# Kernel optimization log

Hardware: AMD Instinct MI355X
Metric: run time of the kernel (lower is better)

The kernel has to match this reference:

```python
import jax, jax.numpy as jnp
import numpy as np
from math import sqrt

B, N, CS, H, D, K = 8, 256, 512, 8, 64, 32
NB = 2 * K + 1          # no_bins = 65
CT = 2048               # c_transition
INF = 1e9
WL = sqrt(0.5)          # w_L
EPS = 1e-5


def setup_inputs() -> dict:
    key = jax.random.key(0)
    ks = jax.random.split(key, 10)
    sc = 0.02
    return {
        "s": jax.random.normal(ks[0], (B, N, CS), jnp.float32),
        "masks": jnp.ones((B, N), jnp.bool_),
        "wq": jax.random.normal(ks[1], (CS, D * H), jnp.float32) * sc,
        "wk": jax.random.normal(ks[2], (CS, D * H), jnp.float32) * sc,
        "wv": jax.random.normal(ks[3], (CS, D * H), jnp.float32) * sc,
        "wb": jax.random.normal(ks[4], (NB, H), jnp.float32) * sc,
        "wo": jax.random.normal(ks[5], ((NB + D) * H, CS), jnp.float32) * sc,
        "bo": jnp.zeros((CS,), jnp.float32),
        "ln1_g": jnp.ones((CS,), jnp.float32),
        "ln1_b": jnp.zeros((CS,), jnp.float32),
        "w1": jax.random.normal(ks[6], (CS, CT), jnp.float32) * sc,
        "b1": jnp.zeros((CT,), jnp.float32),
        "w2": jax.random.normal(ks[7], (CT, CS), jnp.float32) * sc,
        "b2": jnp.zeros((CS,), jnp.float32),
        "ln2_g": jnp.ones((CS,), jnp.float32),
        "ln2_b": jnp.zeros((CS,), jnp.float32),
    }


def _layernorm(x, g, b):
    m = jnp.mean(x, -1, keepdims=True)
    v = jnp.var(x, -1, keepdims=True)
    return (x - m) * jax.lax.rsqrt(v + EPS) * g + b


def _heads(x):  # [B,N,D*H] -> [B,H,N,D]  (torch: reshape(B,N,D,H) then move H forward)
    return jnp.transpose(x.reshape(B, N, D, H), (0, 3, 1, 2))


def reference(s, masks, wq, wk, wv, wb, wo, bo, ln1_g, ln1_b, w1, b1, w2, b2, ln2_g, ln2_b):
    mf = masks.astype(s.dtype)                       # [B,N]
    sq = mf[:, :, None] * mf[:, None, :]             # [B,N,N]

    # relative position one-hot, clipped to [-K, K] -> [N,N,NB]
    r = jnp.arange(N)
    dmat = jnp.clip(r[:, None] - r[None, :], -K, K) + K
    relpos_base = jax.nn.one_hot(dmat, NB, dtype=s.dtype)
    relpos = relpos_base[None] * sq[..., None]       # [B,N,N,NB]

    b_bias = jnp.einsum('bijc,ch->bhij', relpos, wb)  # [B,H,N,N]

    q = _heads(s @ wq)                               # [B,H,N,D]
    k = _heads(s @ wk)
    v = _heads(s @ wv)

    logits = WL * (jnp.einsum('bhid,bhjd->bhij', q, k) / sqrt(D) + b_bias)
    logits = logits - INF * (1.0 - sq)[:, None]      # mask
    a = jax.nn.softmax(logits, axis=-1)              # [B,H,N,N]

    # pairwise aggregation and value aggregation (einsum avoids [B,H,N,N,NB] blowup)
    o_pair = jnp.einsum('bhij,bijc->bhic', a, relpos)  # [B,H,N,NB]
    o = jnp.einsum('bhij,bhjd->bhid', a, v)            # [B,H,N,D]

    op = jnp.transpose(o_pair, (0, 2, 1, 3)).reshape(B, N, H * NB)
    ov = jnp.transpose(o, (0, 2, 1, 3)).reshape(B, N, H * D)
    embd = jnp.concatenate([op, ov], axis=-1) @ wo + bo   # [B,N,CS]

    x = _layernorm(s + embd, ln1_g, ln1_b)
    ff = jax.nn.relu(x @ w1 + b1) @ w2 + b2
    x = _layernorm(x + ff, ln2_g, ln2_b)
    return x, a
```

## Files before the change

### kernel.cpp

```cpp
#include <hip/hip_runtime.h>
#include <hip/hip_bf16.h>
#include <cstdint>

#define B_ 8
#define N_ 256
#define CS_ 512
#define H_ 8
#define D_ 64
#define K_ 32
#define NB_ 65
#define CT_ 2048
#define WL_ 0.70710678118654752f

typedef __attribute__((ext_vector_type(8))) short bf16x8;
typedef __attribute__((ext_vector_type(4))) float f32x4;

#define GLOBAL_AS __attribute__((address_space(1)))
#define LDS_AS __attribute__((address_space(3)))

__device__ __forceinline__ void async16(void* lds, const void* g) {
  __builtin_amdgcn_global_load_lds((const GLOBAL_AS uint32_t*)g,
                                   (LDS_AS uint32_t*)lds, 16, 0, 0);
}

__device__ __forceinline__ ushort f2bf(float v) {
  __hip_bfloat16 hb = __float2bfloat16(v);
  return *(ushort*)&hb;
}

__global__ __launch_bounds__(256) void gemm_bf16(
    const ushort* __restrict__ A, const ushort* __restrict__ Bt,
    const float* __restrict__ bias, float* __restrict__ C,
    ushort* __restrict__ Cb, int M, int Nc, int Kd, int flags) {
  __shared__ ushort As[128 * 64];
  __shared__ ushort Bs[128 * 64];
  int tid = threadIdx.x;
  int bm = blockIdx.y * 128, bn = blockIdx.x * 128;
  int S = gridDim.z, z = blockIdx.z;
  int T = Kd >> 6;
  int it0 = (z * T) / S, it1 = ((z + 1) * T) / S;
  if (flags & 8) C += (size_t)z * M * Nc;
  int w = tid >> 6, l = tid & 63;
  int wr = (w >> 1) * 64, wc = (w & 1) * 64;
  int lm = l & 15, lq = l >> 4;
  int srow = tid >> 3;
  int sg = tid & 7;

  f32x4 acc[4][4];
#pragma unroll
  for (int i = 0; i < 4; ++i)
#pragma unroll
    for (int j = 0; j < 4; ++j) acc[i][j] = (f32x4){0.f, 0.f, 0.f, 0.f};

  for (int it = it0; it < it1; ++it) {
    int k0 = it << 6;
    __syncthreads();
#pragma unroll
    for (int r = 0; r < 4; ++r) {
      int row = r * 32 + srow;
      int gl = sg ^ (row & 7);
      async16(&As[row * 64 + sg * 8],
              A + (size_t)(bm + row) * Kd + k0 + gl * 8);
      async16(&Bs[row * 64 + sg * 8],
              Bt + (size_t)(bn + row) * Kd + k0 + gl * 8);
    }
    __syncthreads();
#pragma unroll
    for (int kk = 0; kk < 2; ++kk) {
      bf16x8 af[4], bfr[4];
#pragma unroll
      for (int i = 0; i < 4; ++i) {
        int ma = wr + 16 * i + lm;
        af[i] = *(const bf16x8*)&As[ma * 64 + ((kk * 4 + lq) ^ (ma & 7)) * 8];
        int nb = wc + 16 * i + lm;
        bfr[i] = *(const bf16x8*)&Bs[nb * 64 + ((kk * 4 + lq) ^ (nb & 7)) * 8];
      }
#pragma unroll
      for (int i = 0; i < 4; ++i)
#pragma unroll
        for (int j = 0; j < 4; ++j)
          acc[i][j] = __builtin_amdgcn_mfma_f32_16x16x32_bf16(
              af[i], bfr[j], acc[i][j], 0, 0, 0);
    }
  }
#pragma unroll
  for (int j = 0; j < 4; ++j) {
    int col = bn + wc + 16 * j + lm;
    float bv = ((flags & 1) && z == 0) ? bias[col] : 0.f;
#pragma unroll
    for (int i = 0; i < 4; ++i) {
#pragma unroll
      for (int r = 0; r < 4; ++r) {
        int row = bm + wr + 16 * i + lq * 4 + r;
        float v = acc[i][j][r] + bv;
        if (flags & 2) v = fmaxf(v, 0.f);
        if (flags & 8) C[(size_t)row * Nc + col] = v;
        if (flags & 4) Cb[(size_t)row * Nc + col] = f2bf(v);
        if (flags & 16) {
          int which = col >> 9, c = col & 511;
          int hh = c >> 6, d2 = c & 63;
          int bb = row >> 8, nn = row & 255;
          size_t dst;
          if (which == 2)
            dst = (size_t)2 * 1048576 + (((size_t)(bb * 8 + hh) * 64) + d2) * 256 + nn;
          else
            dst = (size_t)which * 1048576 + (((size_t)(bb * 8 + hh) * 256) + nn) * 64 + d2;
          Cb[dst] = f2bf(v);
        }
      }
    }
  }
}

__global__ __launch_bounds__(256) void prep_all(
    const float* __restrict__ s, __hip_bfloat16* __restrict__ s_bf,
    const float* __restrict__ wq, const float* __restrict__ wk,
    const float* __restrict__ wv, const float* __restrict__ wo,
    const float* __restrict__ w1, const float* __restrict__ w2,
    __hip_bfloat16* __restrict__ wqkvT, __hip_bfloat16* __restrict__ wopT,
    __hip_bfloat16* __restrict__ w1T, __hip_bfloat16* __restrict__ w2T) {
  int blk = blockIdx.x;
  if (blk < 1024) {
    int i = blk * 256 + threadIdx.x;
    float4 v = ((const float4*)s)[i];
    s_bf[i * 4 + 0] = __float2bfloat16(v.x);
    s_bf[i * 4 + 1] = __float2bfloat16(v.y);
    s_bf[i * 4 + 2] = __float2bfloat16(v.z);
    s_bf[i * 4 + 3] = __float2bfloat16(v.w);
    return;
  }
  blk -= 1024;
  __shared__ float tile[32][33];
  const float* src;
  __hip_bfloat16* dst;
  int R, C, Kpad, tX, tIdx, whichBase = -1;
  if (blk < 768) {
    int zz = blk >> 8; tIdx = blk & 255;
    src = zz == 0 ? wq : zz == 1 ? wk : wv;
    dst = wqkvT; whichBase = zz * 512; R = 512; C = 512; Kpad = 512; tX = 16;
  } else if (blk < 1312) {
    tIdx = blk - 768; src = wo; dst = wopT; R = 1032; C = 512; Kpad = 1088; tX = 16;
  } else if (blk < 2336) {
    tIdx = blk - 1312; src = w1; dst = w1T; R = 512; C = 2048; Kpad = 512; tX = 64;
  } else {
    tIdx = blk - 2336; src = w2; dst = w2T; R = 2048; C = 512; Kpad = 2048; tX = 16;
  }
  int c0 = (tIdx % tX) * 32, r0 = (tIdx / tX) * 32;
  int tx = threadIdx.x & 31, ty = threadIdx.x >> 5;
#pragma unroll
  for (int yy = 0; yy < 32; yy += 8) {
    int r = r0 + ty + yy, c = c0 + tx;
    tile[ty + yy][tx] = (r < R && c < C) ? src[(size_t)r * C + c] : 0.f;
  }
  __syncthreads();
#pragma unroll
  for (int yy = 0; yy < 32; yy += 8) {
    int cc = c0 + ty + yy, k = r0 + tx;
    if (cc < C && k < Kpad) {
      int n = (whichBase >= 0) ? (whichBase + (cc & 7) * 64 + (cc >> 3)) : cc;
      dst[(size_t)n * Kpad + k] = __float2bfloat16(tile[tx][ty + yy]);
    }
  }
}

__global__ __launch_bounds__(256) void attn_fused(
    const ushort* __restrict__ qh, const ushort* __restrict__ kh,
    const ushort* __restrict__ vT, const int* __restrict__ masks,
    const float* __restrict__ wb, float* __restrict__ a_out,
    ushort* __restrict__ cat) {
  int strip = blockIdx.x & 3, bh = blockIdx.x >> 2;
  int h = bh & 7, b = bh >> 3;
  __shared__ ushort lds[20480];
  __shared__ float wbs[NB_];
  __shared__ float mfj[256];
  ushort* Ks = lds;
  ushort* Qs = lds + 16384;
  ushort* Vh = lds;
  ushort* Ps = lds + 8192;
  int tid = threadIdx.x;
  int srow = tid >> 3, sg = tid & 7;
#pragma unroll
  for (int rr = 0; rr < 8; ++rr) {
    int row = rr * 32 + srow;
    int gl = sg ^ (row & 7);
    async16(&Ks[row * 64 + sg * 8],
            kh + ((size_t)bh * 256 + row) * 64 + gl * 8);
  }
#pragma unroll
  for (int rr = 0; rr < 2; ++rr) {
    int row = rr * 32 + srow;
    int gl = sg ^ (row & 7);
    async16(&Qs[row * 64 + sg * 8],
            qh + ((size_t)bh * 256 + strip * 64 + row) * 64 + gl * 8);
  }
  if (tid < NB_) wbs[tid] = wb[tid * H_ + h];
  mfj[tid] = (masks[b * 256 + tid] != 0) ? 1.f : 0.f;
  __syncthreads();

  int w = tid >> 6, l = tid & 63, lm = l & 15, lq = l >> 4;
  bf16x8 qf[2];
#pragma unroll
  for (int kk = 0; kk < 2; ++kk) {
    int qrow = w * 16 + lm;
    qf[kk] = *(const bf16x8*)&Qs[qrow * 64 + ((kk * 4 + lq) ^ (qrow & 7)) * 8];
  }
  f32x4 acc[16];
#pragma unroll
  for (int ct = 0; ct < 16; ++ct) {
    int krow = ct * 16 + lm;
    bf16x8 kf0 = *(const bf16x8*)&Ks[krow * 64 + ((lq) ^ (krow & 7)) * 8];
    bf16x8 kf1 = *(const bf16x8*)&Ks[krow * 64 + ((4 + lq) ^ (krow & 7)) * 8];
    f32x4 zf = (f32x4){0.f, 0.f, 0.f, 0.f};
    zf = __builtin_amdgcn_mfma_f32_16x16x32_bf16(qf[0], kf0, zf, 0, 0, 0);
    acc[ct] = __builtin_amdgcn_mfma_f32_16x16x32_bf16(qf[1], kf1, zf, 0, 0, 0);
  }
  int ibase = strip * 64 + w * 16 + lq * 4;
  float mfi[4];
#pragma unroll
  for (int r = 0; r < 4; ++r) mfi[r] = mfj[ibase + r];
#pragma unroll
  for (int ct = 0; ct < 16; ++ct) {
    int j = ct * 16 + lm;
    float mj = mfj[j];
#pragma unroll
    for (int r = 0; r < 4; ++r) {
      int i = ibase + r;
      int diff = i - j;
      int cb = diff < -K_ ? 0 : (diff > K_ ? 2 * K_ : diff + K_);
      float sq = mfi[r] * mj;
      acc[ct][r] = WL_ * (acc[ct][r] * 0.125f + wbs[cb] * sq) - 1e9f * (1.f - sq);
    }
  }
  float mx[4], sm[4];
#pragma unroll
  for (int r = 0; r < 4; ++r) {
    float m = acc[0][r];
#pragma unroll
    for (int ct = 1; ct < 16; ++ct) m = fmaxf(m, acc[ct][r]);
#pragma unroll
    for (int o = 1; o < 16; o <<= 1) m = fmaxf(m, __shfl_xor(m, o, 64));
    mx[r] = m;
  }
#pragma unroll
  for (int ct = 0; ct < 16; ++ct)
#pragma unroll
    for (int r = 0; r < 4; ++r) acc[ct][r] = __expf(acc[ct][r] - mx[r]);
#pragma unroll
  for (int r = 0; r < 4; ++r) {
    float s = 0.f;
#pragma unroll
    for (int ct = 0; ct < 16; ++ct) s += acc[ct][r];
#pragma unroll
    for (int o = 1; o < 16; o <<= 1) s += __shfl_xor(s, o, 64);
    sm[r] = 1.f / s;
  }
  float p0[4] = {0.f, 0.f, 0.f, 0.f}, p64[4] = {0.f, 0.f, 0.f, 0.f};
#pragma unroll
  for (int ct = 0; ct < 16; ++ct) {
    int j = ct * 16 + lm;
    float mj = mfj[j];
#pragma unroll
    for (int r = 0; r < 4; ++r) {
      int i = ibase + r;
      float aval = acc[ct][r] * sm[r];
      a_out[((size_t)bh * 256 + i) * 256 + j] = aval;
      float val = aval * mfi[r] * mj;
      int diff = i - j;
      if (diff <= -K_)      p0[r] += val;
      else if (diff >= K_)  p64[r] += val;
      else cat[((size_t)(b * 256 + i)) * 1088 + h * 65 + diff + K_] = f2bf(val);
    }
  }
#pragma unroll
  for (int r = 0; r < 4; ++r)
#pragma unroll
    for (int o = 1; o < 16; o <<= 1) {
      p0[r]  += __shfl_xor(p0[r], o, 64);
      p64[r] += __shfl_xor(p64[r], o, 64);
    }
  if (lm == 0) {
#pragma unroll
    for (int r = 0; r < 4; ++r) {
      int i = ibase + r;
      cat[((size_t)(b * 256 + i)) * 1088 + h * 65 + 0]      = f2bf(p0[r]);
      cat[((size_t)(b * 256 + i)) * 1088 + h * 65 + 2 * K_] = f2bf(p64[r]);
    }
  }
#pragma unroll
  for (int r = 0; r < 4; ++r) {
    int i = ibase + r;
#pragma unroll
    for (int t = 0; t < 4; ++t) {
      int c = 1 + lm + 16 * t;
      if (c < 64) {
        int j = i - c + K_;
        if (j < 0 || j > 255)
          cat[((size_t)(b * 256 + i)) * 1088 + h * 65 + c] = 0;
      }
    }
  }
  if (h == 0) {
    for (int idx = tid; idx < 64 * 56; idx += 256) {
      int r = idx / 56, c = 1032 + idx - r * 56 * 1 - (idx / 56) * 0;
      c = 1032 + (idx - r * 56);
      cat[((size_t)(b * 256 + strip * 64 + r)) * 1088 + c] = 0;
    }
  }
  __syncthreads();
  f32x4 acc2[4];
#pragma unroll
  for (int nt = 0; nt < 4; ++nt) acc2[nt] = (f32x4){0.f, 0.f, 0.f, 0.f};
  int vrow_ = tid >> 4, vsg = tid & 15;
#pragma unroll
  for (int hf = 0; hf < 2; ++hf) {
    if (hf == 1) __syncthreads();
#pragma unroll
    for (int rr = 0; rr < 4; ++rr) {
      int d = rr * 16 + vrow_;
      int gl = vsg ^ (d & 7);
      async16(&Vh[d * 128 + vsg * 8],
              vT + (size_t)bh * 16384 + d * 256 + hf * 128 + gl * 8);
    }
#pragma unroll
    for (int cl = 0; cl < 8; ++cl) {
      int ct = hf * 8 + cl;
#pragma unroll
      for (int r = 0; r < 4; ++r) {
        int rowl = w * 16 + lq * 4 + r;
        float aval = acc[ct][r] * sm[r];
        int g = cl * 2 + (lm >> 3);
        Ps[rowl * 128 + ((g ^ (rowl & 7)) << 3) + (lm & 7)] = f2bf(aval);
      }
    }
    __syncthreads();
#pragma unroll
    for (int kst = 0; kst < 4; ++kst) {
      int prow = w * 16 + lm;
      bf16x8 af = *(const bf16x8*)&Ps[prow * 128 + (((kst * 4 + lq) ^ (prow & 7)) << 3)];
#pragma unroll
      for (int nt = 0; nt < 4; ++nt) {
        int d = nt * 16 + lm;
        bf16x8 bfr = *(const bf16x8*)&Vh[d * 128 + (((kst * 4 + lq) ^ (d & 7)) << 3)];
        acc2[nt] = __builtin_amdgcn_mfma_f32_16x16x32_bf16(af, bfr, acc2[nt], 0, 0, 0);
      }
    }
  }
#pragma unroll
  for (int nt = 0; nt < 4; ++nt) {
    int d = nt * 16 + lm;
#pragma unroll
    for (int r = 0; r < 4; ++r) {
      int i = ibase + r;
      cat[((size_t)(b * 256 + i)) * 1088 + 520 + h * 64 + d] = f2bf(acc2[nt][r]);
    }
  }
}

__device__ __forceinline__ float lnReduceSum(float v, float* red) {
#pragma unroll
  for (int o = 32; o > 0; o >>= 1) v += __shfl_xor(v, o, 64);
  int w = threadIdx.x >> 6;
  __syncthreads();
  if ((threadIdx.x & 63) == 0) red[w] = v;
  __syncthreads();
  return red[0] + red[1] + red[2] + red[3];
}

__global__ __launch_bounds__(256) void ln_sum(
    const float* __restrict__ x1, const float* __restrict__ xp,
    int S, int stride, const float* __restrict__ g,
    const float* __restrict__ bta, float* __restrict__ out,
    __hip_bfloat16* __restrict__ out_bf) {
  __shared__ float red[4];
  int row = blockIdx.x, tid = threadIdx.x;
  size_t base = (size_t)row * 512;
  float v0 = x1[base + tid];
  float v1 = x1[base + tid + 256];
  for (int s = 0; s < S; ++s) {
    v0 += xp[(size_t)s * stride + base + tid];
    v1 += xp[(size_t)s * stride + base + tid + 256];
  }
  float su = lnReduceSum(v0 + v1, red);
  float sq = lnReduceSum(v0 * v0 + v1 * v1, red);
  float mean = su * (1.f / 512.f);
  float var = sq * (1.f / 512.f) - mean * mean;
  float inv = rsqrtf(var + 1e-5f);
  float o0 = (v0 - mean) * inv * g[tid] + bta[tid];
  float o1 = (v1 - mean) * inv * g[tid + 256] + bta[tid + 256];
  out[base + tid]       = o0;
  out[base + tid + 256] = o1;
  if (out_bf) {
    out_bf[base + tid]       = __float2bfloat16(o0);
    out_bf[base + tid + 256] = __float2bfloat16(o1);
  }
}

extern "C" void kernel_launch(void* const* d_in, const int* in_sizes, int n_in,
                              void* d_out, int out_size, void* d_ws, size_t ws_size,
                              hipStream_t stream) {
  const float* s     = (const float*)d_in[0];
  const int*   masks = (const int*)d_in[1];
  const float* wq = (const float*)d_in[2];
  const float* wk = (const float*)d_in[3];
  const float* wv = (const float*)d_in[4];
  const float* wb = (const float*)d_in[5];
  const float* wo = (const float*)d_in[6];
  const float* bo = (const float*)d_in[7];
  const float* ln1_g = (const float*)d_in[8];
  const float* ln1_b = (const float*)d_in[9];
  const float* w1 = (const float*)d_in[10];
  const float* b1 = (const float*)d_in[11];
  const float* w2 = (const float*)d_in[12];
  const float* b2 = (const float*)d_in[13];
  const float* ln2_g = (const float*)d_in[14];
  const float* ln2_b = (const float*)d_in[15];

  float* out_x = (float*)d_out;
  float* out_a = out_x + 1048576;

  float* ws = (float*)d_ws;
  float* embd_part = ws + 0;
  float* xbuf      = ws + 4194304;
  float* ff_part   = ws + 5242880;
  ushort* qkv_bf   = (ushort*)(ws + 9437184);
  ushort* q_bf = qkv_bf;
  ushort* k_bf = qkv_bf + 1048576;
  ushort* v_bf = qkv_bf + 2097152;
  ushort* cat_bf = (ushort*)(ws + 10223616);
  __hip_bfloat16* h_bf  = (__hip_bfloat16*)(ws + 11337728);
  __hip_bfloat16* s_bf  = (__hip_bfloat16*)(ws + 13434880);
  __hip_bfloat16* x_bf  = (__hip_bfloat16*)(ws + 13959168);
  __hip_bfloat16* wqkvT = (__hip_bfloat16*)(ws + 14483456);
  __hip_bfloat16* wopT  = (__hip_bfloat16*)(ws + 14876672);
  __hip_bfloat16* w1T   = (__hip_bfloat16*)(ws + 15155200);
  __hip_bfloat16* w2T   = (__hip_bfloat16*)(ws + 15679488);

  dim3 blk(256);
  prep_all<<<dim3(4384), blk, 0, stream>>>(s, s_bf, wq, wk, wv, wo, w1, w2,
                                           wqkvT, wopT, w1T, w2T);
  gemm_bf16<<<dim3(12, 16, 1), blk, 0, stream>>>(
      (const ushort*)s_bf, (const ushort*)wqkvT, nullptr, nullptr,
      qkv_bf, 2048, 1536, 512, 16);
  attn_fused<<<dim3(256), blk, 0, stream>>>(q_bf, k_bf, v_bf, masks, wb,
                                            out_a, cat_bf);
  gemm_bf16<<<dim3(4, 16, 4), blk, 0, stream>>>(
      cat_bf, (const ushort*)wopT, bo, embd_part, nullptr,
      2048, 512, 1088, 1 | 8);
  ln_sum<<<dim3(2048), blk, 0, stream>>>(s, embd_part, 4, 1048576,
                                         ln1_g, ln1_b, xbuf, x_bf);
  gemm_bf16<<<dim3(16, 16, 1), blk, 0, stream>>>(
      (const ushort*)x_bf, (const ushort*)w1T, b1, nullptr, (ushort*)h_bf,
      2048, 2048, 512, 1 | 2 | 4);
  gemm_bf16<<<dim3(4, 16, 4), blk, 0, stream>>>(
      (const ushort*)h_bf, (const ushort*)w2T, b2, ff_part, nullptr,
      2048, 512, 2048, 1 | 8);
  ln_sum<<<dim3(2048), blk, 0, stream>>>(xbuf, ff_part, 4, 1048576,
                                         ln2_g, ln2_b, out_x, nullptr);
}
```

Baseline: 197.1 us.

## Shrink GEMM tiles to 64x128 with two waves; load Q/V fragments directly into registers

```diff
diff --git a/kernel.cpp b/kernel.cpp
--- a/kernel.cpp
+++ b/kernel.cpp
@@ -28,20 +28,19 @@
   return *(ushort*)&hb;
 }
 
-__global__ __launch_bounds__(256) void gemm_bf16(
+__global__ __launch_bounds__(128) void gemm_bf16(
     const ushort* __restrict__ A, const ushort* __restrict__ Bt,
     const float* __restrict__ bias, float* __restrict__ C,
     ushort* __restrict__ Cb, int M, int Nc, int Kd, int flags) {
-  __shared__ ushort As[128 * 64];
+  __shared__ ushort As[64 * 64];
   __shared__ ushort Bs[128 * 64];
   int tid = threadIdx.x;
-  int bm = blockIdx.y * 128, bn = blockIdx.x * 128;
+  int bm = blockIdx.y * 64, bn = blockIdx.x * 128;
   int S = gridDim.z, z = blockIdx.z;
   int T = Kd >> 6;
   int it0 = (z * T) / S, it1 = ((z + 1) * T) / S;
   if (flags & 8) C += (size_t)z * M * Nc;
   int w = tid >> 6, l = tid & 63;
-  int wr = (w >> 1) * 64, wc = (w & 1) * 64;
   int lm = l & 15, lq = l >> 4;
   int srow = tid >> 3;
   int sg = tid & 7;
@@ -57,10 +56,15 @@
     __syncthreads();
 #pragma unroll
     for (int r = 0; r < 4; ++r) {
-      int row = r * 32 + srow;
+      int row = r * 16 + srow;
       int gl = sg ^ (row & 7);
       async16(&As[row * 64 + sg * 8],
               A + (size_t)(bm + row) * Kd + k0 + gl * 8);
+    }
+#pragma unroll
+    for (int r = 0; r < 8; ++r) {
+      int row = r * 16 + srow;
+      int gl = sg ^ (row & 7);
       async16(&Bs[row * 64 + sg * 8],
               Bt + (size_t)(bn + row) * Kd + k0 + gl * 8);
     }
@@ -70,9 +74,9 @@
       bf16x8 af[4], bfr[4];
 #pragma unroll
       for (int i = 0; i < 4; ++i) {
-        int ma = wr + 16 * i + lm;
+        int ma = 16 * i + lm;
         af[i] = *(const bf16x8*)&As[ma * 64 + ((kk * 4 + lq) ^ (ma & 7)) * 8];
-        int nb = wc + 16 * i + lm;
+        int nb = w * 64 + 16 * i + lm;
         bfr[i] = *(const bf16x8*)&Bs[nb * 64 + ((kk * 4 + lq) ^ (nb & 7)) * 8];
       }
 #pragma unroll
@@ -85,13 +89,13 @@
   }
 #pragma unroll
   for (int j = 0; j < 4; ++j) {
-    int col = bn + wc + 16 * j + lm;
+    int col = bn + w * 64 + 16 * j + lm;
     float bv = ((flags & 1) && z == 0) ? bias[col] : 0.f;
 #pragma unroll
     for (int i = 0; i < 4; ++i) {
 #pragma unroll
       for (int r = 0; r < 4; ++r) {
-        int row = bm + wr + 16 * i + lq * 4 + r;
+        int row = bm + 16 * i + lq * 4 + r;
         float v = acc[i][j][r] + bv;
         if (flags & 2) v = fmaxf(v, 0.f);
         if (flags & 8) C[(size_t)row * Nc + col] = v;
@@ -170,13 +174,10 @@
     ushort* __restrict__ cat) {
   int strip = blockIdx.x & 3, bh = blockIdx.x >> 2;
   int h = bh & 7, b = bh >> 3;
-  __shared__ ushort lds[20480];
+  __shared__ ushort Ks[256 * 64];
+  __shared__ ushort Ps[64 * 64];
   __shared__ float wbs[NB_];
   __shared__ float mfj[256];
-  ushort* Ks = lds;
-  ushort* Qs = lds + 16384;
-  ushort* Vh = lds;
-  ushort* Ps = lds + 8192;
   int tid = threadIdx.x;
   int srow = tid >> 3, sg = tid & 7;
 #pragma unroll
@@ -186,24 +187,18 @@
     async16(&Ks[row * 64 + sg * 8],
             kh + ((size_t)bh * 256 + row) * 64 + gl * 8);
   }
-#pragma unroll
-  for (int rr = 0; rr < 2; ++rr) {
-    int row = rr * 32 + srow;
-    int gl = sg ^ (row & 7);
-    async16(&Qs[row * 64 + sg * 8],
-            qh + ((size_t)bh * 256 + strip * 64 + row) * 64 + gl * 8);
+  int w = tid >> 6, l = tid & 63, lm = l & 15, lq = l >> 4;
+  bf16x8 qf[2];
+  {
+    const ushort* qrow =
+        qh + ((size_t)bh * 256 + strip * 64 + w * 16 + lm) * 64 + lq * 8;
+    qf[0] = *(const bf16x8*)qrow;
+    qf[1] = *(const bf16x8*)(qrow + 32);
   }
   if (tid < NB_) wbs[tid] = wb[tid * H_ + h];
   mfj[tid] = (masks[b * 256 + tid] != 0) ? 1.f : 0.f;
   __syncthreads();
 
-  int w = tid >> 6, l = tid & 63, lm = l & 15, lq = l >> 4;
-  bf16x8 qf[2];
-#pragma unroll
-  for (int kk = 0; kk < 2; ++kk) {
-    int qrow = w * 16 + lm;
-    qf[kk] = *(const bf16x8*)&Qs[qrow * 64 + ((kk * 4 + lq) ^ (qrow & 7)) * 8];
-  }
   f32x4 acc[16];
 #pragma unroll
   for (int ct = 0; ct < 16; ++ct) {
@@ -301,48 +296,42 @@
   }
   if (h == 0) {
     for (int idx = tid; idx < 64 * 56; idx += 256) {
-      int r = idx / 56, c = 1032 + idx - r * 56 * 1 - (idx / 56) * 0;
-      c = 1032 + (idx - r * 56);
+      int r = idx / 56, c = 1032 + (idx - r * 56);
       cat[((size_t)(b * 256 + strip * 64 + r)) * 1088 + c] = 0;
     }
   }
-  __syncthreads();
   f32x4 acc2[4];
 #pragma unroll
   for (int nt = 0; nt < 4; ++nt) acc2[nt] = (f32x4){0.f, 0.f, 0.f, 0.f};
-  int vrow_ = tid >> 4, vsg = tid & 15;
-#pragma unroll
-  for (int hf = 0; hf < 2; ++hf) {
-    if (hf == 1) __syncthreads();
-#pragma unroll
-    for (int rr = 0; rr < 4; ++rr) {
-      int d = rr * 16 + vrow_;
-      int gl = vsg ^ (d & 7);
-      async16(&Vh[d * 128 + vsg * 8],
-              vT + (size_t)bh * 16384 + d * 256 + hf * 128 + gl * 8);
-    }
-#pragma unroll
-    for (int cl = 0; cl < 8; ++cl) {
-      int ct = hf * 8 + cl;
+  const ushort* vbase = vT + (size_t)bh * 16384;
+#pragma unroll
+  for (int qt = 0; qt < 4; ++qt) {
+    bf16x8 vf0[4], vf1[4];
+#pragma unroll
+    for (int nt = 0; nt < 4; ++nt) {
+      const ushort* vrow = vbase + (size_t)(nt * 16 + lm) * 256 + qt * 64 + lq * 8;
+      vf0[nt] = *(const bf16x8*)vrow;
+      vf1[nt] = *(const bf16x8*)(vrow + 32);
+    }
+#pragma unroll
+    for (int ctl = 0; ctl < 4; ++ctl) {
+      int ct = qt * 4 + ctl;
 #pragma unroll
       for (int r = 0; r < 4; ++r) {
         int rowl = w * 16 + lq * 4 + r;
-        float aval = acc[ct][r] * sm[r];
-        int g = cl * 2 + (lm >> 3);
-        Ps[rowl * 128 + ((g ^ (rowl & 7)) << 3) + (lm & 7)] = f2bf(aval);
+        int g = ctl * 2 + (lm >> 3);
+        Ps[rowl * 64 + ((g ^ (rowl & 7)) << 3) + (lm & 7)] =
+            f2bf(acc[ct][r] * sm[r]);
       }
     }
-    __syncthreads();
-#pragma unroll
-    for (int kst = 0; kst < 4; ++kst) {
-      int prow = w * 16 + lm;
-      bf16x8 af = *(const bf16x8*)&Ps[prow * 128 + (((kst * 4 + lq) ^ (prow & 7)) << 3)];
-#pragma unroll
-      for (int nt = 0; nt < 4; ++nt) {
-        int d = nt * 16 + lm;
-        bf16x8 bfr = *(const bf16x8*)&Vh[d * 128 + (((kst * 4 + lq) ^ (d & 7)) << 3)];
-        acc2[nt] = __builtin_amdgcn_mfma_f32_16x16x32_bf16(af, bfr, acc2[nt], 0, 0, 0);
-      }
+    int prow = w * 16 + lm;
+#pragma unroll
+    for (int kst = 0; kst < 2; ++kst) {
+      bf16x8 af = *(const bf16x8*)&Ps[prow * 64 + (((kst * 4 + lq) ^ (prow & 7)) << 3)];
+#pragma unroll
+      for (int nt = 0; nt < 4; ++nt)
+        acc2[nt] = __builtin_amdgcn_mfma_f32_16x16x32_bf16(
+            af, kst ? vf1[nt] : vf0[nt], acc2[nt], 0, 0, 0);
     }
   }
 #pragma unroll
@@ -435,23 +424,23 @@
   __hip_bfloat16* w1T   = (__hip_bfloat16*)(ws + 15155200);
   __hip_bfloat16* w2T   = (__hip_bfloat16*)(ws + 15679488);
 
-  dim3 blk(256);
+  dim3 blk(256), blkg(128);
   prep_all<<<dim3(4384), blk, 0, stream>>>(s, s_bf, wq, wk, wv, wo, w1, w2,
                                            wqkvT, wopT, w1T, w2T);
-  gemm_bf16<<<dim3(12, 16, 1), blk, 0, stream>>>(
+  gemm_bf16<<<dim3(12, 32, 1), blkg, 0, stream>>>(
       (const ushort*)s_bf, (const ushort*)wqkvT, nullptr, nullptr,
       qkv_bf, 2048, 1536, 512, 16);
   attn_fused<<<dim3(256), blk, 0, stream>>>(q_bf, k_bf, v_bf, masks, wb,
                                             out_a, cat_bf);
-  gemm_bf16<<<dim3(4, 16, 4), blk, 0, stream>>>(
+  gemm_bf16<<<dim3(4, 32, 4), blkg, 0, stream>>>(
       cat_bf, (const ushort*)wopT, bo, embd_part, nullptr,
       2048, 512, 1088, 1 | 8);
   ln_sum<<<dim3(2048), blk, 0, stream>>>(s, embd_part, 4, 1048576,
                                          ln1_g, ln1_b, xbuf, x_bf);
-  gemm_bf16<<<dim3(16, 16, 1), blk, 0, stream>>>(
+  gemm_bf16<<<dim3(16, 32, 1), blkg, 0, stream>>>(
       (const ushort*)x_bf, (const ushort*)w1T, b1, nullptr, (ushort*)h_bf,
       2048, 2048, 512, 1 | 2 | 4);
-  gemm_bf16<<<dim3(4, 16, 4), blk, 0, stream>>>(
+  gemm_bf16<<<dim3(4, 32, 4), blkg, 0, stream>>>(
       (const ushort*)h_bf, (const ushort*)w2T, b2, ff_part, nullptr,
       2048, 512, 2048, 1 | 8);
   ln_sum<<<dim3(2048), blk, 0, stream>>>(xbuf, ff_part, 4, 1048576,
```

Result: no change. 194.7 us (-1.2%).
